# Optimization experiments

Hardware: AMD Instinct MI355X
Metric: run time of the kernel (lower is better)

The kernel has to match this reference:

```python
import jax, jax.numpy as jnp
import numpy as np

C, H, W, NC, LC = 512, 160, 160, 1203, 64


def setup_inputs() -> dict:
    key = jax.random.key(0)
    ks = jax.random.split(key, 8)
    return {
        "cls_feat": jax.random.normal(ks[0], (1, C, H, W), jnp.float32),
        "loc_feat": jax.random.normal(ks[1], (1, LC, H, W), jnp.float32),
        "conf": jax.random.uniform(ks[2], (1,), jnp.float32, 0.2, 0.8),
        "pf_w": jax.random.normal(ks[3], (C,), jnp.float32) * 0.02,   # pf 1x1 conv, C->1
        "pf_b": jnp.zeros((1,), jnp.float32),
        "vocab_w": jax.random.normal(ks[4], (NC, C), jnp.float32) * 0.02,  # conv2linear weight
        "vocab_b": jnp.zeros((NC,), jnp.float32),
        "loc_w": jax.random.normal(ks[5], (LC, LC), jnp.float32) * 0.02,   # loc 1x1 conv
        "loc_b": jnp.zeros((LC,), jnp.float32),
    }


def reference(cls_feat, loc_feat, conf, pf_w, pf_b, vocab_w, vocab_b, loc_w, loc_b):
    B, Cc, Hh, Ww = cls_feat.shape
    # proposal-filter score: 1x1 conv C->1 on batch 0, flattened to [HW]
    pf_score = jnp.einsum('c,chw->hw', pf_w, cls_feat[0]).reshape(-1) + pf_b  # [HW]
    mask = jax.nn.sigmoid(pf_score) > conf[0]  # [HW] bool
    # tokens: [1, HW, C]
    tok = cls_feat.reshape(B, Cc, Hh * Ww).transpose(0, 2, 1)
    # static-shape equivalent of the proposal filter: zero masked-out tokens
    tok = tok * mask[None, :, None].astype(tok.dtype)
    # vocab linear (converted 1x1 conv): [1, HW, NC] -> [1, NC, HW]
    cls_out = (jnp.einsum('bnc,vc->bnv', tok, vocab_w) + vocab_b).transpose(0, 2, 1)
    # localization 1x1 conv
    loc_out = jnp.einsum('oi,bihw->bohw', loc_w, loc_feat) + loc_b[None, :, None, None]
    return loc_out, cls_out, mask
```

## Files before the change

kernel.cpp:

```cpp
#include <hip/hip_runtime.h>
#include <math.h>


constexpr int C_   = 512;
constexpr int HW_  = 25600;
constexpr int NC_  = 1203;
constexpr int VPAD_ = 1216;

constexpr int LOC_OFF_  = 0;
constexpr int CLS_OFF_  = 64 * HW_;
constexpr int MASK_OFF_ = CLS_OFF_ + NC_ * HW_;

constexpr int PF_BLOCKS_    = HW_ / 64;
constexpr int LOC_BLOCKS_   = 400;
constexpr int FILL_BLOCKS_  = 2048;
constexpr int TRANS_BLOCKS_ = 19 * 8;

typedef float vfloat4 __attribute__((ext_vector_type(4)));

__global__ void k_init(int* cnt) { *cnt = 0; }

__global__ __launch_bounds__(256) void k_main(
    const float* __restrict__ cls_feat, const float* __restrict__ loc_feat,
    const float* __restrict__ conf, const float* __restrict__ pf_w,
    const float* __restrict__ pf_b, const float* __restrict__ vocab_w,
    const float* __restrict__ vocab_b, const float* __restrict__ loc_w,
    const float* __restrict__ loc_b, float* __restrict__ out,
    int* __restrict__ cnt, int* __restrict__ idxList,
    float* __restrict__ AT4, int jcap)
{
    const int bid = blockIdx.x;
    const int tid = threadIdx.x;

    if (bid < PF_BLOCKS_) {
        __shared__ double sPart[256];
        const int hwi   = tid & 63;
        const int slice = tid >> 6;
        const int hw    = bid * 64 + hwi;
        const float* p  = cls_feat + (size_t)slice * 128 * HW_ + hw;
        const float* w  = pf_w + slice * 128;
        double acc = 0.0;
        #pragma unroll 4
        for (int k = 0; k < 128; ++k)
            acc += (double)w[k] * (double)p[(size_t)k * HW_];
        sPart[tid] = acc;
        __syncthreads();
        if (slice == 0) {
            double s = sPart[hwi] + sPart[64 + hwi] + sPart[128 + hwi] +
                       sPart[192 + hwi] + (double)pf_b[0];
            double sig = 1.0 / (1.0 + exp(-s));
            bool m = sig > (double)conf[0];
            out[MASK_OFF_ + hw] = m ? 1.0f : 0.0f;
            if (m) {
                int pos = atomicAdd(cnt, 1);
                if (pos < HW_) idxList[pos] = hw;
            }
        }
    } else if (bid < PF_BLOCKS_ + LOC_BLOCKS_) {
        const int j   = bid - PF_BLOCKS_;
        const int hwb = j % 100;
        const int o0  = (j / 100) * 16;
        __shared__ float sw[16][64];
        for (int i = tid; i < 16 * 64; i += 256)
            sw[i >> 6][i & 63] = loc_w[(o0 + (i >> 6)) * 64 + (i & 63)];
        __syncthreads();
        const int hw = hwb * 256 + tid;
        float acc[16];
        #pragma unroll
        for (int r = 0; r < 16; ++r) acc[r] = loc_b[o0 + r];
        for (int i = 0; i < 64; ++i) {
            float f = loc_feat[(size_t)i * HW_ + hw];
            #pragma unroll
            for (int r = 0; r < 16; ++r) acc[r] += sw[r][i] * f;
        }
        #pragma unroll
        for (int r = 0; r < 16; ++r)
            out[LOC_OFF_ + (size_t)(o0 + r) * HW_ + hw] = acc[r];
    } else if (bid < PF_BLOCKS_ + LOC_BLOCKS_ + FILL_BLOCKS_) {
        const int fb = bid - PF_BLOCKS_ - LOC_BLOCKS_;
        const int total4 = NC_ * HW_ / 4;
        vfloat4* o = (vfloat4*)(out + CLS_OFF_);
        for (int i = fb * 256 + tid; i < total4; i += FILL_BLOCKS_ * 256) {
            int v = i / (HW_ / 4);
            float b = vocab_b[v];
            vfloat4 val = {b, b, b, b};
            __builtin_nontemporal_store(val, &o[i]);
        }
    } else {
        if (jcap <= 0) return;
        const int tb = bid - PF_BLOCKS_ - LOC_BLOCKS_ - FILL_BLOCKS_;
        const int v0 = (tb % 19) * 64;
        const int k0 = (tb / 19) * 64;
        __shared__ float t[64][65];
        const int c  = tid & 63;
        const int r4 = tid >> 6;
        #pragma unroll
        for (int i = 0; i < 16; ++i) {
            const int r = r4 * 16 + i;
            const int v = v0 + r;
            t[r][c] = (v < NC_) ? vocab_w[(size_t)v * C_ + k0 + c] : 0.f;
        }
        __syncthreads();
        #pragma unroll
        for (int i = 0; i < 16; ++i) {
            const int k  = r4 * 16 + i;
            const int kg = k0 + k;
            AT4[((size_t)(kg >> 2) * VPAD_ + v0 + c) * 4 + (kg & 3)] = t[c][k];
        }
    }
}

__global__ __launch_bounds__(256) void k_gatherJ(
    const float* __restrict__ cls_feat, const int* __restrict__ cnt,
    const int* __restrict__ idxList, float* __restrict__ BdT, int jcap)
{
    const int count = min(*cnt, HW_);
    if (count > jcap) return;
    const int t = threadIdx.x;
    for (int j = blockIdx.x; j < count; j += gridDim.x) {
        const int hw = idxList[j];
        BdT[(size_t)j * C_ + t]       = cls_feat[(size_t)t * HW_ + hw];
        BdT[(size_t)j * C_ + 256 + t] = cls_feat[(size_t)(256 + t) * HW_ + hw];
    }
}

__global__ __launch_bounds__(256) void k_gemm6(
    const float* __restrict__ AT4, const float* __restrict__ vocab_b,
    const int* __restrict__ cnt, const int* __restrict__ idxList,
    const float* __restrict__ BdT, float* __restrict__ out, int jcap)
{
    const int count = min(*cnt, HW_);
    if (count == 0 || count > jcap) return;
    const int jBase = blockIdx.y * 4;
    if (jBase >= count) return;

    const int tid  = threadIdx.x;
    const int lane = tid & 63;
    const int w    = __builtin_amdgcn_readfirstlane(tid >> 6);
    const int v0   = blockIdx.x * 64;
    const int v    = v0 + lane;
    const float* __restrict__ Acol = AT4 + (size_t)v * 4;

    const int j0 = jBase + 0, j1 = jBase + 1, j2 = jBase + 2, j3 = jBase + 3;
    const float* __restrict__ B0 = BdT + (size_t)(j0 < count ? j0 : 0) * C_;
    const float* __restrict__ B1 = BdT + (size_t)(j1 < count ? j1 : 0) * C_;
    const float* __restrict__ B2 = BdT + (size_t)(j2 < count ? j2 : 0) * C_;
    const float* __restrict__ B3 = BdT + (size_t)(j3 < count ? j3 : 0) * C_;

    vfloat4 ac0 = {0,0,0,0}, ac1 = {0,0,0,0}, ac2 = {0,0,0,0}, ac3 = {0,0,0,0};

    const int kqBeg = w * 32;
    #pragma unroll 8
    for (int q = 0; q < 32; ++q) {
        const int kq = kqBeg + q;
        const vfloat4 a = *(const vfloat4*)(Acol + (size_t)kq * VPAD_ * 4);
        const vfloat4 b0 = *(const vfloat4*)(B0 + kq * 4);
        const vfloat4 b1 = *(const vfloat4*)(B1 + kq * 4);
        const vfloat4 b2 = *(const vfloat4*)(B2 + kq * 4);
        const vfloat4 b3 = *(const vfloat4*)(B3 + kq * 4);
        ac0 += a * b0;
        ac1 += a * b1;
        ac2 += a * b2;
        ac3 += a * b3;
    }

    __shared__ float sRed[4][4][64];
    sRed[w][0][lane] = (ac0.x + ac0.y) + (ac0.z + ac0.w);
    sRed[w][1][lane] = (ac1.x + ac1.y) + (ac1.z + ac1.w);
    sRed[w][2][lane] = (ac2.x + ac2.y) + (ac2.z + ac2.w);
    sRed[w][3][lane] = (ac3.x + ac3.y) + (ac3.z + ac3.w);
    __syncthreads();

    if (tid < 64 && v < NC_) {
        const float bias = vocab_b[v];
        #pragma unroll
        for (int jj = 0; jj < 4; ++jj) {
            const int j = jBase + jj;
            if (j < count) {
                const float s =
                    (sRed[0][jj][lane] + sRed[1][jj][lane]) +
                    (sRed[2][jj][lane] + sRed[3][jj][lane]);
                const int hw = idxList[j];
                out[CLS_OFF_ + (size_t)v * HW_ + hw] = s + bias;
            }
        }
    }
}

__global__ __launch_bounds__(256) void k_gemm_fallback(
    const float* __restrict__ cls_feat, const float* __restrict__ vocab_w,
    const float* __restrict__ vocab_b, const int* __restrict__ cnt,
    const int* __restrict__ idxList, float* __restrict__ out, int capB)
{
    const int count = min(*cnt, HW_);
    if (count <= capB) return;
    const int v0 = blockIdx.x * 64;

    __shared__ float sAT[16][64];
    __shared__ float sBT[16][64];
    __shared__ int   sIdx[64];

    const int tid = threadIdx.x;
    const int tx = tid & 15;
    const int ty = tid >> 4;
    const int r  = tid >> 2;
    const int kq = tid & 3;

    for (int jb = blockIdx.y; (jb << 6) < count; jb += gridDim.y) {
        const int j0 = jb << 6;
        __syncthreads();
        if (tid < 64) {
            int j = j0 + tid;
            sIdx[tid] = (j < count) ? idxList[j] : -1;
        }
        __syncthreads();
        const int hwj = sIdx[r];

        float acc[4][4] = {};
        for (int k0 = 0; k0 < C_; k0 += 16) {
            float4 a4 = make_float4(0.f, 0.f, 0.f, 0.f);
            if (v0 + r < NC_)
                a4 = *(const float4*)(vocab_w + (size_t)(v0 + r) * C_ + k0 + kq * 4);
            float b0 = 0.f, b1 = 0.f, b2 = 0.f, b3 = 0.f;
            if (hwj >= 0) {
                const float* bp = cls_feat + (size_t)(k0 + kq * 4) * HW_ + hwj;
                b0 = bp[0]; b1 = bp[HW_]; b2 = bp[2 * HW_]; b3 = bp[3 * HW_];
            }
            __syncthreads();
            sAT[kq * 4 + 0][r] = a4.x; sAT[kq * 4 + 1][r] = a4.y;
            sAT[kq * 4 + 2][r] = a4.z; sAT[kq * 4 + 3][r] = a4.w;
            sBT[kq * 4 + 0][r] = b0;   sBT[kq * 4 + 1][r] = b1;
            sBT[kq * 4 + 2][r] = b2;   sBT[kq * 4 + 3][r] = b3;
            __syncthreads();
            #pragma unroll
            for (int kk = 0; kk < 16; ++kk) {
                const float4 av = *(const float4*)&sAT[kk][ty * 4];
                const float4 bv = *(const float4*)&sBT[kk][tx * 4];
                acc[0][0] += av.x * bv.x; acc[0][1] += av.x * bv.y;
                acc[0][2] += av.x * bv.z; acc[0][3] += av.x * bv.w;
                acc[1][0] += av.y * bv.x; acc[1][1] += av.y * bv.y;
                acc[1][2] += av.y * bv.z; acc[1][3] += av.y * bv.w;
                acc[2][0] += av.z * bv.x; acc[2][1] += av.z * bv.y;
                acc[2][2] += av.z * bv.z; acc[2][3] += av.z * bv.w;
                acc[3][0] += av.w * bv.x; acc[3][1] += av.w * bv.y;
                acc[3][2] += av.w * bv.z; acc[3][3] += av.w * bv.w;
            }
        }
        #pragma unroll
        for (int a = 0; a < 4; ++a) {
            int v = v0 + ty * 4 + a;
            if (v >= NC_) continue;
            float bias = vocab_b[v];
            #pragma unroll
            for (int b = 0; b < 4; ++b) {
                int j = j0 + tx * 4 + b;
                if (j < count) {
                    int hw = sIdx[tx * 4 + b];
                    out[CLS_OFF_ + (size_t)v * HW_ + hw] = acc[a][b] + bias;
                }
            }
        }
    }
}

extern "C" void kernel_launch(void* const* d_in, const int* in_sizes, int n_in,
                              void* d_out, int out_size, void* d_ws,
                              size_t ws_size, hipStream_t stream) {
    const float* cls_feat = (const float*)d_in[0];
    const float* loc_feat = (const float*)d_in[1];
    const float* conf     = (const float*)d_in[2];
    const float* pf_w     = (const float*)d_in[3];
    const float* pf_b     = (const float*)d_in[4];
    const float* vocab_w  = (const float*)d_in[5];
    const float* vocab_b  = (const float*)d_in[6];
    const float* loc_w    = (const float*)d_in[7];
    const float* loc_b    = (const float*)d_in[8];
    float* out = (float*)d_out;

    int*   cnt     = (int*)d_ws;
    int*   idxList = (int*)((char*)d_ws + 4096);
    size_t fixed   = 4096 + (size_t)HW_ * sizeof(int);
    size_t atBytes = (size_t)(C_ / 4) * VPAD_ * 4 * sizeof(float);
    float* AT4     = (float*)((char*)d_ws + fixed);
    float* BdT     = (float*)((char*)d_ws + fixed + atBytes);

    int jcap = 0;
    if (ws_size > fixed + atBytes) {
        size_t cols = (ws_size - fixed - atBytes) / ((size_t)C_ * sizeof(float));
        jcap = (int)(cols > 1024 ? 1024 : cols);
        jcap &= ~63;
    }

    hipLaunchKernelGGL(k_init, dim3(1), dim3(1), 0, stream, cnt);
    hipLaunchKernelGGL(k_main,
                       dim3(PF_BLOCKS_ + LOC_BLOCKS_ + FILL_BLOCKS_ +
                            TRANS_BLOCKS_),
                       dim3(256), 0, stream,
                       cls_feat, loc_feat, conf, pf_w, pf_b, vocab_w, vocab_b,
                       loc_w, loc_b, out, cnt, idxList, AT4, jcap);
    if (jcap > 0) {
        hipLaunchKernelGGL(k_gatherJ, dim3(512), dim3(256), 0, stream,
                           cls_feat, cnt, idxList, BdT, jcap);
        hipLaunchKernelGGL(k_gemm6, dim3(19, jcap / 4), dim3(256), 0, stream,
                           AT4, vocab_b, cnt, idxList, BdT, out, jcap);
    }
    hipLaunchKernelGGL(k_gemm_fallback, dim3((NC_ + 63) / 64, 8), dim3(256),
                       0, stream, cls_feat, vocab_w, vocab_b, cnt, idxList,
                       out, jcap);
}
```

Measured before the change: 62.92 us.

## Overlap sparse vocab GEMM with fill and loc conv in one kernel, then scatter

Splits the old fused kernel so the proposal-filter and weight transpose run first. The sparse GEMM, the loc 1x1 conv and the bias fill of the class output then run together in one kernel, with GEMM results written to a dense temporary buffer. A final scatter kernel writes the temporary results into the class output at the selected positions once the fill has finished. The aim is to hide the large bias-fill store traffic behind GEMM and loc compute, at the cost of an extra launch, an extra round trip through the temporary buffer, and a fixed workspace requirement for jcap=1024.

Measured after the change: 68.71 us. +9.2%, slower.

```diff
diff --git a/kernel.cpp b/kernel.cpp
--- a/kernel.cpp
+++ b/kernel.cpp
@@ -2,9 +2,9 @@
 #include <math.h>
 
 
-constexpr int C_   = 512;
-constexpr int HW_  = 25600;
-constexpr int NC_  = 1203;
+constexpr int C_    = 512;
+constexpr int HW_   = 25600;
+constexpr int NC_   = 1203;
 constexpr int VPAD_ = 1216;
 
 constexpr int LOC_OFF_  = 0;
@@ -12,20 +12,19 @@
 constexpr int MASK_OFF_ = CLS_OFF_ + NC_ * HW_;
 
 constexpr int PF_BLOCKS_    = HW_ / 64;
+constexpr int TRANS_BLOCKS_ = 19 * 8;
+constexpr int GEMM_BLOCKS_  = 19 * 256;
 constexpr int LOC_BLOCKS_   = 400;
 constexpr int FILL_BLOCKS_  = 2048;
-constexpr int TRANS_BLOCKS_ = 19 * 8;
 
 typedef float vfloat4 __attribute__((ext_vector_type(4)));
 
 __global__ void k_init(int* cnt) { *cnt = 0; }
 
-__global__ __launch_bounds__(256) void k_main(
-    const float* __restrict__ cls_feat, const float* __restrict__ loc_feat,
-    const float* __restrict__ conf, const float* __restrict__ pf_w,
-    const float* __restrict__ pf_b, const float* __restrict__ vocab_w,
-    const float* __restrict__ vocab_b, const float* __restrict__ loc_w,
-    const float* __restrict__ loc_b, float* __restrict__ out,
+__global__ __launch_bounds__(256) void k_pre(
+    const float* __restrict__ cls_feat, const float* __restrict__ conf,
+    const float* __restrict__ pf_w, const float* __restrict__ pf_b,
+    const float* __restrict__ vocab_w, float* __restrict__ out,
     int* __restrict__ cnt, int* __restrict__ idxList,
     float* __restrict__ AT4, int jcap)
 {
@@ -56,8 +55,107 @@
                 if (pos < HW_) idxList[pos] = hw;
             }
         }
-    } else if (bid < PF_BLOCKS_ + LOC_BLOCKS_) {
-        const int j   = bid - PF_BLOCKS_;
+    } else {
+        if (jcap <= 0) return;
+        const int tb = bid - PF_BLOCKS_;
+        const int v0 = (tb % 19) * 64;
+        const int k0 = (tb / 19) * 64;
+        __shared__ float t[64][65];
+        const int c  = tid & 63;
+        const int r4 = tid >> 6;
+        #pragma unroll
+        for (int i = 0; i < 16; ++i) {
+            const int r = r4 * 16 + i;
+            const int v = v0 + r;
+            t[r][c] = (v < NC_) ? vocab_w[(size_t)v * C_ + k0 + c] : 0.f;
+        }
+        __syncthreads();
+        #pragma unroll
+        for (int i = 0; i < 16; ++i) {
+            const int k  = r4 * 16 + i;
+            const int kg = k0 + k;
+            AT4[((size_t)(kg >> 2) * VPAD_ + v0 + c) * 4 + (kg & 3)] = t[c][k];
+        }
+    }
+}
+
+__global__ __launch_bounds__(256) void k_gatherJ(
+    const float* __restrict__ cls_feat, const int* __restrict__ cnt,
+    const int* __restrict__ idxList, float* __restrict__ BdT, int jcap)
+{
+    const int count = min(*cnt, HW_);
+    if (count > jcap) return;
+    const int t = threadIdx.x;
+    for (int j = blockIdx.x; j < count; j += gridDim.x) {
+        const int hw = idxList[j];
+        BdT[(size_t)j * C_ + t]       = cls_feat[(size_t)t * HW_ + hw];
+        BdT[(size_t)j * C_ + 256 + t] = cls_feat[(size_t)(256 + t) * HW_ + hw];
+    }
+}
+
+__global__ __launch_bounds__(256) void k_mega(
+    const float* __restrict__ loc_feat, const float* __restrict__ vocab_b,
+    const float* __restrict__ loc_w, const float* __restrict__ loc_b,
+    const float* __restrict__ AT4, const int* __restrict__ cnt,
+    const float* __restrict__ BdT, float* __restrict__ clsTmp,
+    float* __restrict__ out, int jcap)
+{
+    const int bid = blockIdx.x;
+    const int tid = threadIdx.x;
+
+    if (bid < GEMM_BLOCKS_) {
+        const int count = min(*cnt, HW_);
+        if (count == 0 || count > jcap) return;
+        const int jBase = (bid / 19) * 4;
+        if (jBase >= count) return;
+
+        const int lane = tid & 63;
+        const int w    = __builtin_amdgcn_readfirstlane(tid >> 6);
+        const int v0   = (bid % 19) * 64;
+        const int v    = v0 + lane;
+        const float* __restrict__ Acol = AT4 + (size_t)v * 4;
+
+        const int j0 = jBase + 0, j1 = jBase + 1, j2 = jBase + 2, j3 = jBase + 3;
+        const float* __restrict__ B0 = BdT + (size_t)(j0 < count ? j0 : 0) * C_;
+        const float* __restrict__ B1 = BdT + (size_t)(j1 < count ? j1 : 0) * C_;
+        const float* __restrict__ B2 = BdT + (size_t)(j2 < count ? j2 : 0) * C_;
+        const float* __restrict__ B3 = BdT + (size_t)(j3 < count ? j3 : 0) * C_;
+
+        vfloat4 ac0 = {0,0,0,0}, ac1 = {0,0,0,0}, ac2 = {0,0,0,0}, ac3 = {0,0,0,0};
+        const int kqBeg = w * 32;
+        #pragma unroll 8
+        for (int q = 0; q < 32; ++q) {
+            const int kq = kqBeg + q;
+            const vfloat4 a  = *(const vfloat4*)(Acol + (size_t)kq * VPAD_ * 4);
+            const vfloat4 b0 = *(const vfloat4*)(B0 + kq * 4);
+            const vfloat4 b1 = *(const vfloat4*)(B1 + kq * 4);
+            const vfloat4 b2 = *(const vfloat4*)(B2 + kq * 4);
+            const vfloat4 b3 = *(const vfloat4*)(B3 + kq * 4);
+            ac0 += a * b0; ac1 += a * b1; ac2 += a * b2; ac3 += a * b3;
+        }
+
+        __shared__ float sRed[4][4][64];
+        sRed[w][0][lane] = (ac0.x + ac0.y) + (ac0.z + ac0.w);
+        sRed[w][1][lane] = (ac1.x + ac1.y) + (ac1.z + ac1.w);
+        sRed[w][2][lane] = (ac2.x + ac2.y) + (ac2.z + ac2.w);
+        sRed[w][3][lane] = (ac3.x + ac3.y) + (ac3.z + ac3.w);
+        __syncthreads();
+
+        if (tid < 64) {
+            const float bias = (v < NC_) ? vocab_b[v] : 0.f;
+            #pragma unroll
+            for (int jj = 0; jj < 4; ++jj) {
+                const int j = jBase + jj;
+                if (j < count) {
+                    const float s =
+                        (sRed[0][jj][lane] + sRed[1][jj][lane]) +
+                        (sRed[2][jj][lane] + sRed[3][jj][lane]);
+                    clsTmp[(size_t)j * VPAD_ + v] = s + bias;
+                }
+            }
+        }
+    } else if (bid < GEMM_BLOCKS_ + LOC_BLOCKS_) {
+        const int j   = bid - GEMM_BLOCKS_;
         const int hwb = j % 100;
         const int o0  = (j / 100) * 16;
         __shared__ float sw[16][64];
@@ -76,8 +174,8 @@
         #pragma unroll
         for (int r = 0; r < 16; ++r)
             out[LOC_OFF_ + (size_t)(o0 + r) * HW_ + hw] = acc[r];
-    } else if (bid < PF_BLOCKS_ + LOC_BLOCKS_ + FILL_BLOCKS_) {
-        const int fb = bid - PF_BLOCKS_ - LOC_BLOCKS_;
+    } else {
+        const int fb = bid - GEMM_BLOCKS_ - LOC_BLOCKS_;
         const int total4 = NC_ * HW_ / 4;
         vfloat4* o = (vfloat4*)(out + CLS_OFF_);
         for (int i = fb * 256 + tid; i < total4; i += FILL_BLOCKS_ * 256) {
@@ -86,105 +184,21 @@
             vfloat4 val = {b, b, b, b};
             __builtin_nontemporal_store(val, &o[i]);
         }
-    } else {
-        if (jcap <= 0) return;
-        const int tb = bid - PF_BLOCKS_ - LOC_BLOCKS_ - FILL_BLOCKS_;
-        const int v0 = (tb % 19) * 64;
-        const int k0 = (tb / 19) * 64;
-        __shared__ float t[64][65];
-        const int c  = tid & 63;
-        const int r4 = tid >> 6;
-        #pragma unroll
-        for (int i = 0; i < 16; ++i) {
-            const int r = r4 * 16 + i;
-            const int v = v0 + r;
-            t[r][c] = (v < NC_) ? vocab_w[(size_t)v * C_ + k0 + c] : 0.f;
-        }
-        __syncthreads();
-        #pragma unroll
-        for (int i = 0; i < 16; ++i) {
-            const int k  = r4 * 16 + i;
-            const int kg = k0 + k;
-            AT4[((size_t)(kg >> 2) * VPAD_ + v0 + c) * 4 + (kg & 3)] = t[c][k];
-        }
-    }
-}
-
-__global__ __launch_bounds__(256) void k_gatherJ(
-    const float* __restrict__ cls_feat, const int* __restrict__ cnt,
-    const int* __restrict__ idxList, float* __restrict__ BdT, int jcap)
+    }
+}
+
+__global__ __launch_bounds__(256) void k_scatter(
+    const int* __restrict__ cnt, const int* __restrict__ idxList,
+    const float* __restrict__ clsTmp, float* __restrict__ out, int jcap)
 {
     const int count = min(*cnt, HW_);
     if (count > jcap) return;
-    const int t = threadIdx.x;
-    for (int j = blockIdx.x; j < count; j += gridDim.x) {
-        const int hw = idxList[j];
-        BdT[(size_t)j * C_ + t]       = cls_feat[(size_t)t * HW_ + hw];
-        BdT[(size_t)j * C_ + 256 + t] = cls_feat[(size_t)(256 + t) * HW_ + hw];
-    }
-}
-
-__global__ __launch_bounds__(256) void k_gemm6(
-    const float* __restrict__ AT4, const float* __restrict__ vocab_b,
-    const int* __restrict__ cnt, const int* __restrict__ idxList,
-    const float* __restrict__ BdT, float* __restrict__ out, int jcap)
-{
-    const int count = min(*cnt, HW_);
-    if (count == 0 || count > jcap) return;
-    const int jBase = blockIdx.y * 4;
-    if (jBase >= count) return;
-
-    const int tid  = threadIdx.x;
-    const int lane = tid & 63;
-    const int w    = __builtin_amdgcn_readfirstlane(tid >> 6);
-    const int v0   = blockIdx.x * 64;
-    const int v    = v0 + lane;
-    const float* __restrict__ Acol = AT4 + (size_t)v * 4;
-
-    const int j0 = jBase + 0, j1 = jBase + 1, j2 = jBase + 2, j3 = jBase + 3;
-    const float* __restrict__ B0 = BdT + (size_t)(j0 < count ? j0 : 0) * C_;
-    const float* __restrict__ B1 = BdT + (size_t)(j1 < count ? j1 : 0) * C_;
-    const float* __restrict__ B2 = BdT + (size_t)(j2 < count ? j2 : 0) * C_;
-    const float* __restrict__ B3 = BdT + (size_t)(j3 < count ? j3 : 0) * C_;
-
-    vfloat4 ac0 = {0,0,0,0}, ac1 = {0,0,0,0}, ac2 = {0,0,0,0}, ac3 = {0,0,0,0};
-
-    const int kqBeg = w * 32;
-    #pragma unroll 8
-    for (int q = 0; q < 32; ++q) {
-        const int kq = kqBeg + q;
-        const vfloat4 a = *(const vfloat4*)(Acol + (size_t)kq * VPAD_ * 4);
-        const vfloat4 b0 = *(const vfloat4*)(B0 + kq * 4);
-        const vfloat4 b1 = *(const vfloat4*)(B1 + kq * 4);
-        const vfloat4 b2 = *(const vfloat4*)(B2 + kq * 4);
-        const vfloat4 b3 = *(const vfloat4*)(B3 + kq * 4);
-        ac0 += a * b0;
-        ac1 += a * b1;
-        ac2 += a * b2;
-        ac3 += a * b3;
-    }
-
-    __shared__ float sRed[4][4][64];
-    sRed[w][0][lane] = (ac0.x + ac0.y) + (ac0.z + ac0.w);
-    sRed[w][1][lane] = (ac1.x + ac1.y) + (ac1.z + ac1.w);
-    sRed[w][2][lane] = (ac2.x + ac2.y) + (ac2.z + ac2.w);
-    sRed[w][3][lane] = (ac3.x + ac3.y) + (ac3.z + ac3.w);
-    __syncthreads();
-
-    if (tid < 64 && v < NC_) {
-        const float bias = vocab_b[v];
-        #pragma unroll
-        for (int jj = 0; jj < 4; ++jj) {
-            const int j = jBase + jj;
-            if (j < count) {
-                const float s =
-                    (sRed[0][jj][lane] + sRed[1][jj][lane]) +
-                    (sRed[2][jj][lane] + sRed[3][jj][lane]);
-                const int hw = idxList[j];
-                out[CLS_OFF_ + (size_t)v * HW_ + hw] = s + bias;
-            }
-        }
-    }
+    const int j = blockIdx.x;
+    if (j >= count) return;
+    const int hw = idxList[j];
+    const float* __restrict__ src = clsTmp + (size_t)j * VPAD_;
+    for (int v = threadIdx.x; v < NC_; v += 256)
+        out[CLS_OFF_ + (size_t)v * HW_ + hw] = src[v];
 }
 
 __global__ __launch_bounds__(256) void k_gemm_fallback(
@@ -277,32 +291,36 @@
     const float* loc_b    = (const float*)d_in[8];
     float* out = (float*)d_out;
 
-    int*   cnt     = (int*)d_ws;
-    int*   idxList = (int*)((char*)d_ws + 4096);
-    size_t fixed   = 4096 + (size_t)HW_ * sizeof(int);
-    size_t atBytes = (size_t)(C_ / 4) * VPAD_ * 4 * sizeof(float);
-    float* AT4     = (float*)((char*)d_ws + fixed);
-    float* BdT     = (float*)((char*)d_ws + fixed + atBytes);
+    int*   cnt      = (int*)d_ws;
+    int*   idxList  = (int*)((char*)d_ws + 4096);
+    size_t fixed    = 4096 + (size_t)HW_ * sizeof(int);
+    size_t atBytes  = (size_t)(C_ / 4) * VPAD_ * 4 * sizeof(float);
+    size_t bdtBytes = (size_t)1024 * C_ * sizeof(float);
+    size_t tmpBytes = (size_t)1024 * VPAD_ * sizeof(float);
+    float* AT4      = (float*)((char*)d_ws + fixed);
+    float* BdT      = (float*)((char*)d_ws + fixed + atBytes);
+    float* clsTmp   = (float*)((char*)d_ws + fixed + atBytes + bdtBytes);
 
     int jcap = 0;
-    if (ws_size > fixed + atBytes) {
-        size_t cols = (ws_size - fixed - atBytes) / ((size_t)C_ * sizeof(float));
-        jcap = (int)(cols > 1024 ? 1024 : cols);
-        jcap &= ~63;
-    }
+    if (ws_size >= fixed + atBytes + bdtBytes + tmpBytes) jcap = 1024;
 
     hipLaunchKernelGGL(k_init, dim3(1), dim3(1), 0, stream, cnt);
-    hipLaunchKernelGGL(k_main,
-                       dim3(PF_BLOCKS_ + LOC_BLOCKS_ + FILL_BLOCKS_ +
-                            TRANS_BLOCKS_),
-                       dim3(256), 0, stream,
-                       cls_feat, loc_feat, conf, pf_w, pf_b, vocab_w, vocab_b,
-                       loc_w, loc_b, out, cnt, idxList, AT4, jcap);
+    hipLaunchKernelGGL(k_pre, dim3(PF_BLOCKS_ + TRANS_BLOCKS_), dim3(256),
+                       0, stream,
+                       cls_feat, conf, pf_w, pf_b, vocab_w, out, cnt,
+                       idxList, AT4, jcap);
     if (jcap > 0) {
         hipLaunchKernelGGL(k_gatherJ, dim3(512), dim3(256), 0, stream,
                            cls_feat, cnt, idxList, BdT, jcap);
-        hipLaunchKernelGGL(k_gemm6, dim3(19, jcap / 4), dim3(256), 0, stream,
-                           AT4, vocab_b, cnt, idxList, BdT, out, jcap);
+    }
+    hipLaunchKernelGGL(k_mega,
+                       dim3(GEMM_BLOCKS_ + LOC_BLOCKS_ + FILL_BLOCKS_),
+                       dim3(256), 0, stream,
+                       loc_feat, vocab_b, loc_w, loc_b, AT4, cnt, BdT,
+                       clsTmp, out, jcap);
+    if (jcap > 0) {
+        hipLaunchKernelGGL(k_scatter, dim3(1024), dim3(256), 0, stream,
+                           cnt, idxList, clsTmp, out, jcap);
     }
     hipLaunchKernelGGL(k_gemm_fallback, dim3((NC_ + 63) / 64, 8), dim3(256),
                        0, stream, cls_feat, vocab_w, vocab_b, cnt, idxList,
```
